# Optimization experiments

Hardware: AMD Instinct MI355X
Metric: run time of the kernel (lower is better)

Reference implementation:

```python
import jax, jax.numpy as jnp
import numpy as np

B, T, IN, H, OUT = 512, 1000, 39, 64, 48


def setup_inputs() -> dict:
    key = jax.random.key(0)
    ks = jax.random.split(key, 7)
    s = 1.0 / np.sqrt(H)
    return {
        "x": jax.random.normal(ks[0], (B, T, IN), dtype=jnp.float32),
        "W_ih": jax.random.uniform(ks[1], (4 * H, IN), minval=-s, maxval=s, dtype=jnp.float32),
        "W_hh": jax.random.uniform(ks[2], (4 * H, H), minval=-s, maxval=s, dtype=jnp.float32),
        "b_ih": jax.random.uniform(ks[3], (4 * H,), minval=-s, maxval=s, dtype=jnp.float32),
        "b_hh": jax.random.uniform(ks[4], (4 * H,), minval=-s, maxval=s, dtype=jnp.float32),
        "W_out": jax.random.uniform(ks[5], (OUT, H), minval=-s, maxval=s, dtype=jnp.float32),
        "b_out": jax.random.uniform(ks[6], (OUT,), minval=-s, maxval=s, dtype=jnp.float32),
    }


def reference(x, W_ih, W_hh, b_ih, b_hh, W_out, b_out):
    # Single-layer batch-first LSTM (zero init state) + per-step Linear + sigmoid.
    b = b_ih + b_hh  # [4H]
    # Precompute input projections for all timesteps at once: [T, B, 4H]
    xg = jnp.einsum('bti,gi->tbg', x, W_ih) + b

    def step(carry, xg_t):
        h, c = carry
        gates = xg_t + h @ W_hh.T  # [B, 4H], gate order i, f, g, o
        i, f, g, o = jnp.split(gates, 4, axis=-1)
        c = jax.nn.sigmoid(f) * c + jax.nn.sigmoid(i) * jnp.tanh(g)
        h = jax.nn.sigmoid(o) * jnp.tanh(c)
        y = jax.nn.sigmoid(h @ W_out.T + b_out)  # [B, OUT]
        return (h, c), y

    h0 = jnp.zeros((x.shape[0], W_hh.shape[1]), dtype=x.dtype)
    (_, _), ys = jax.lax.scan(step, (h0, h0), xg)  # ys: [T, B, OUT]
    return jnp.swapaxes(ys, 0, 1)  # [B, T, OUT]
```

## Files before the change

kernel.cpp:

```cpp
#include <hip/hip_runtime.h>


#define BB 512
#define TT 1000
#define INF 39
#define HH 64
#define OUTF 48
#define G4 (4 * HH)

#define Q10(M) M(0) M(1) M(2) M(3) M(4) M(5) M(6) M(7) M(8) M(9)
#define Q16(M) M(0) M(1) M(2) M(3) M(4) M(5) M(6) M(7) \
               M(8) M(9) M(10) M(11) M(12) M(13) M(14) M(15)

#define PIN4(v) asm volatile("" : "+v"(v.x), "+v"(v.y), "+v"(v.z), "+v"(v.w));

__global__ __attribute__((amdgpu_waves_per_eu(2, 2)))
__launch_bounds__(256) void lstm_fused_kernel(
    const float* __restrict__ x,
    const float* __restrict__ W_ih,
    const float* __restrict__ W_hh,
    const float* __restrict__ b_ih,
    const float* __restrict__ b_hh,
    const float* __restrict__ W_out,
    const float* __restrict__ b_out,
    float* __restrict__ out)
{
    const int b = blockIdx.x;
    const int tid = threadIdx.x;

    __shared__ float xs[40];
    __shared__ float hs[HH];
    __shared__ float act[G4];

    const float* wih_ptr = W_ih + tid * INF;
#define LOAD_IH4(q) float4 wiq##q; \
    wiq##q.x = wih_ptr[4*(q)]; \
    wiq##q.y = (4*(q)+1 < INF) ? wih_ptr[4*(q)+1] : 0.f; \
    wiq##q.z = (4*(q)+2 < INF) ? wih_ptr[4*(q)+2] : 0.f; \
    wiq##q.w = (4*(q)+3 < INF) ? wih_ptr[4*(q)+3] : 0.f;
    Q10(LOAD_IH4)

    const float4* wh4p = (const float4*)(W_hh + tid * HH);
#define LOAD_HH4(i) float4 wh##i = wh4p[i];
    Q16(LOAD_HH4)

    float bias = b_ih[tid] + b_hh[tid];

    const int o = tid >> 2;
    const int p = tid & 3;
    float4 wo0, wo1, wo2, wo3;
    float bo = 0.f;
    if (tid < 4 * OUTF) {
        const float4* wop = (const float4*)(W_out + o * HH + p * 16);
        wo0 = wop[0]; wo1 = wop[1]; wo2 = wop[2]; wo3 = wop[3];
        bo = b_out[o];
    } else {
        wo0 = wo1 = wo2 = wo3 = make_float4(0.f, 0.f, 0.f, 0.f);
    }

#define PIN_IH(q) PIN4(wiq##q)
    Q10(PIN_IH)
#define PIN_HH(i) PIN4(wh##i)
    Q16(PIN_HH)
    PIN4(wo0) PIN4(wo1) PIN4(wo2) PIN4(wo3)
    asm volatile("" : "+v"(bias), "+v"(bo));

    float c = 0.f;
    const size_t x_base = (size_t)b * TT * INF;
    const size_t out_base = (size_t)b * TT * OUTF;

    if (tid < HH) hs[tid] = 0.f;
    if (tid < INF) xs[tid] = x[x_base + tid];
    if (tid == 39) xs[39] = 0.f;
    float xreg = (tid < INF) ? x[x_base + INF + tid] : 0.f;

    const int gate_type = tid >> 6;
    __syncthreads();

    const float4* xs4 = (const float4*)xs;
    const float4* hs4 = (const float4*)hs;

    for (int t = 0; t < TT; ++t) {
        float a0 = bias, a1 = 0.f, a2 = 0.f, a3 = 0.f;
#define FMA_IH4(q) { const float4 xv = xs4[q]; \
        a0 += xv.x * wiq##q.x; a1 += xv.y * wiq##q.y; \
        a2 += xv.z * wiq##q.z; a3 += xv.w * wiq##q.w; }
        Q10(FMA_IH4)
#define FMA_HH4(i) { const float4 hv = hs4[i]; \
        a0 += hv.x * wh##i.x; a1 += hv.y * wh##i.y; \
        a2 += hv.z * wh##i.z; a3 += hv.w * wh##i.w; }
        Q16(FMA_HH4)
        const float acc = (a0 + a1) + (a2 + a3);

        float a;
        if (gate_type == 2) {
            a = 2.f / (1.f + __expf(-2.f * acc)) - 1.f;
        } else {
            a = 1.f / (1.f + __expf(-acc));
        }
        act[tid] = a;
        __syncthreads();

        if (tid < INF) {
            xs[tid] = xreg;
            if (t + 2 < TT) xreg = x[x_base + (size_t)(t + 2) * INF + tid];
        }
        if (tid < HH) {
            const float ig = act[tid];
            const float fg = act[HH + tid];
            const float gg = act[2 * HH + tid];
            const float og = act[3 * HH + tid];
            c = fg * c + ig * gg;
            const float th = 2.f / (1.f + __expf(-2.f * c)) - 1.f;
            hs[tid] = og * th;
        }
        __syncthreads();

        if (tid < 4 * OUTF) {
            const float4 h0 = hs4[p * 4 + 0];
            const float4 h1 = hs4[p * 4 + 1];
            const float4 h2 = hs4[p * 4 + 2];
            const float4 h3 = hs4[p * 4 + 3];
            float s0 = h0.x * wo0.x + h0.y * wo0.y + h0.z * wo0.z + h0.w * wo0.w;
            float s1 = h1.x * wo1.x + h1.y * wo1.y + h1.z * wo1.z + h1.w * wo1.w;
            float s2 = h2.x * wo2.x + h2.y * wo2.y + h2.z * wo2.z + h2.w * wo2.w;
            float s3 = h3.x * wo3.x + h3.y * wo3.y + h3.z * wo3.z + h3.w * wo3.w;
            float s = (s0 + s1) + (s2 + s3);
            s += __shfl_xor(s, 1, 64);
            s += __shfl_xor(s, 2, 64);
            if (p == 0) {
                const float y = 1.f / (1.f + __expf(-(s + bo)));
                __builtin_nontemporal_store(y, &out[out_base + (size_t)t * OUTF + o]);
            }
        }
    }
}

extern "C" void kernel_launch(void* const* d_in, const int* in_sizes, int n_in,
                              void* d_out, int out_size, void* d_ws, size_t ws_size,
                              hipStream_t stream) {
    const float* x     = (const float*)d_in[0];
    const float* W_ih  = (const float*)d_in[1];
    const float* W_hh  = (const float*)d_in[2];
    const float* b_ih  = (const float*)d_in[3];
    const float* b_hh  = (const float*)d_in[4];
    const float* W_out = (const float*)d_in[5];
    const float* b_out = (const float*)d_in[6];
    float* out = (float*)d_out;

    lstm_fused_kernel<<<dim3(BB), dim3(G4), 0, stream>>>(
        x, W_ih, W_hh, b_ih, b_hh, W_out, b_out, out);
}
```

Before: 1.080 ms.

## Broadcast hidden state via readlane and read x directly from global

Each lane now loads one element of h from shared memory, and the wave broadcasts the values to SGPRs with readlane, replacing 16 float4 LDS reads per step. The x staging buffer in shared memory and its register prefetch are removed. Every thread instead reads the 39 x values for the step straight from global memory with uniform addresses, which should become scalar loads. This cuts LDS traffic but puts global load latency on the per-step critical path. The launch bound attribute also changes to __launch_bounds__(256, 2).

```diff
diff --git a/kernel.cpp b/kernel.cpp
--- a/kernel.cpp
+++ b/kernel.cpp
@@ -14,8 +14,7 @@
 
 #define PIN4(v) asm volatile("" : "+v"(v.x), "+v"(v.y), "+v"(v.z), "+v"(v.w));
 
-__global__ __attribute__((amdgpu_waves_per_eu(2, 2)))
-__launch_bounds__(256) void lstm_fused_kernel(
+__global__ __launch_bounds__(256, 2) void lstm_fused_kernel(
     const float* __restrict__ x,
     const float* __restrict__ W_ih,
     const float* __restrict__ W_hh,
@@ -27,8 +26,8 @@
 {
     const int b = blockIdx.x;
     const int tid = threadIdx.x;
+    const int lane = tid & 63;
 
-    __shared__ float xs[40];
     __shared__ float hs[HH];
     __shared__ float act[G4];
 
@@ -70,26 +69,30 @@
     const size_t out_base = (size_t)b * TT * OUTF;
 
     if (tid < HH) hs[tid] = 0.f;
-    if (tid < INF) xs[tid] = x[x_base + tid];
-    if (tid == 39) xs[39] = 0.f;
-    float xreg = (tid < INF) ? x[x_base + INF + tid] : 0.f;
-
     const int gate_type = tid >> 6;
     __syncthreads();
 
-    const float4* xs4 = (const float4*)xs;
     const float4* hs4 = (const float4*)hs;
 
     for (int t = 0; t < TT; ++t) {
+        const int hbits = __float_as_int(hs[lane]);
+
+        const float* xp = x + x_base + (size_t)t * INF;
+#define XF(k) ((k) < INF ? xp[k] : 0.f)
+
         float a0 = bias, a1 = 0.f, a2 = 0.f, a3 = 0.f;
-#define FMA_IH4(q) { const float4 xv = xs4[q]; \
-        a0 += xv.x * wiq##q.x; a1 += xv.y * wiq##q.y; \
-        a2 += xv.z * wiq##q.z; a3 += xv.w * wiq##q.w; }
-        Q10(FMA_IH4)
-#define FMA_HH4(i) { const float4 hv = hs4[i]; \
-        a0 += hv.x * wh##i.x; a1 += hv.y * wh##i.y; \
-        a2 += hv.z * wh##i.z; a3 += hv.w * wh##i.w; }
-        Q16(FMA_HH4)
+#define HFMA(i) { \
+        a0 += __int_as_float(__builtin_amdgcn_readlane(hbits, 4*(i)+0)) * wh##i.x; \
+        a1 += __int_as_float(__builtin_amdgcn_readlane(hbits, 4*(i)+1)) * wh##i.y; \
+        a2 += __int_as_float(__builtin_amdgcn_readlane(hbits, 4*(i)+2)) * wh##i.z; \
+        a3 += __int_as_float(__builtin_amdgcn_readlane(hbits, 4*(i)+3)) * wh##i.w; }
+        Q16(HFMA)
+#define XFMA(q) { \
+        a0 += XF(4*(q)+0) * wiq##q.x; \
+        a1 += XF(4*(q)+1) * wiq##q.y; \
+        a2 += XF(4*(q)+2) * wiq##q.z; \
+        a3 += XF(4*(q)+3) * wiq##q.w; }
+        Q10(XFMA)
         const float acc = (a0 + a1) + (a2 + a3);
 
         float a;
@@ -101,10 +104,6 @@
         act[tid] = a;
         __syncthreads();
 
-        if (tid < INF) {
-            xs[tid] = xreg;
-            if (t + 2 < TT) xreg = x[x_base + (size_t)(t + 2) * INF + tid];
-        }
         if (tid < HH) {
             const float ig = act[tid];
             const float fg = act[HH + tid];
```

After: 1.474 ms. +36.4%, slower.
